# Kernel optimization log

Measured on AMD Instinct MI355X. Metric: run time of the kernel, lower is better.

## Reference

```python
import jax, jax.numpy as jnp
import numpy as np

D = 512       # d_model
M = 64        # working memory_dim
SE = 32       # episodic slots
SS = 64       # semantic slots
H = 4         # episodic heads
B, L = 2, 1024
BOT = max(D // 4, 32)  # controller bottleneck = 128


def _layernorm(x, g, b, eps=1e-5):
    mu = jnp.mean(x, axis=-1, keepdims=True)
    var = jnp.var(x, axis=-1, keepdims=True)
    return (x - mu) * jax.lax.rsqrt(var + eps) * g + b


def setup_inputs() -> dict:
    key = jax.random.key(0)
    ks = jax.random.split(key, 24)
    r = lambda i, shape, s=0.02: jax.random.normal(ks[i], shape, dtype=jnp.float32) * s
    return {
        "x": jax.random.normal(ks[0], (B, L, D), dtype=jnp.float32),
        # WorkingMemory (weights stored as (in, out))
        "Wq": r(1, (D, M)), "Wk": r(2, (D, M)), "Wv": r(3, (D, D)),
        "Wf": r(4, (D, M)), "bf": jnp.zeros((M,), jnp.float32),
        "Wo": r(5, (D, D)),
        "ln_g": jnp.ones((D,), jnp.float32), "ln_b": jnp.zeros((D,), jnp.float32),
        # EpisodicMemory
        "eslots": r(6, (1, SE, D)),
        "Eq": r(7, (D, D)), "Ek": r(8, (D, D)), "Ev": r(9, (D, D)), "Eo": r(10, (D, D)),
        # SemanticMemory
        "know": r(11, (1, SS, D)),
        "Sin": r(12, (D, D)),
        "Sg_w": r(13, (D, D)), "Sg_b": jnp.zeros((D,), jnp.float32),
        "So": r(14, (D, D)),
        # MemoryController
        "C1w": r(15, (D, BOT)), "C1b": jnp.zeros((BOT,), jnp.float32),
        "C2w": r(16, (BOT, 3)), "C2b": jnp.zeros((3,), jnp.float32),
    }


def _forward(x, Wq, Wk, Wv, Wf, bf, Wo, ln_g, ln_b,
             eslots, Eq, Ek, Ev, Eo,
             know, Sin, Sg_w, Sg_b, So,
             C1w, C1b, C2w, C2b):
    b, l, d = x.shape
    # ---- WorkingMemory (parallel gated linear attention) ----
    scale = M ** -0.5
    q = (jax.nn.elu(x @ Wq) + 1.0) * scale          # (B,L,M)
    k = jax.nn.elu(x @ Wk) + 1.0                    # (B,L,M)
    v = x @ Wv                                      # (B,L,D)
    forget = jax.nn.sigmoid(x @ Wf + bf)            # (B,L,M)
    log_f_cum = jnp.clip(jnp.cumsum(jnp.log(jnp.clip(forget, 1e-6, None)), axis=1), -20.0, 20.0)
    exp_neg = jnp.exp(-log_f_cum)
    exp_pos = jnp.exp(log_f_cum)
    kv = k[..., :, None] * v[..., None, :]          # (B,L,M,D) outer product
    cum_kv = jnp.cumsum(exp_neg[..., None] * kv, axis=1)
    Mstate = exp_pos[..., None] * cum_kv            # (B,L,M,D)
    z = exp_pos * jnp.cumsum(exp_neg * k, axis=1)   # (B,L,M)
    num = jnp.einsum('blm,blmd->bld', q, Mstate)
    den = jnp.einsum('blm,blm->bl', q, z)[..., None] + 1e-6
    w_out = _layernorm(num / den, ln_g, ln_b) @ Wo  # (B,L,D)

    # ---- EpisodicMemory (cross-attn to learned slots) ----
    hd = D // H
    mem = jnp.broadcast_to(eslots, (b, SE, D))
    qh = (x @ Eq).reshape(b, l, H, hd)
    kh = (mem @ Ek).reshape(b, SE, H, hd)
    vh = (mem @ Ev).reshape(b, SE, H, hd)
    scores = jnp.einsum('blhe,bshe->bhls', qh, kh) / jnp.sqrt(jnp.float32(hd))
    attn = jax.nn.softmax(scores, axis=-1)
    e_out = jnp.einsum('bhls,bshe->blhe', attn, vh).reshape(b, l, D) @ Eo

    # ---- SemanticMemory (single-head attn to knowledge, gated residual) ----
    kb = jnp.broadcast_to(know, (b, SS, D))
    qs = x @ Sin                                    # (B,L,D)
    s_scores = jnp.einsum('bld,bsd->bls', qs, kb) / jnp.sqrt(jnp.float32(D))
    s_attn = jax.nn.softmax(s_scores, axis=-1)
    retrieved = jnp.einsum('bls,bsd->bld', s_attn, kb)
    gate = jax.nn.sigmoid(x @ Sg_w + Sg_b)
    s_out = (gate * retrieved + (1.0 - gate) * x) @ So

    # ---- Controller fusion ----
    wts = jax.nn.softmax(jax.nn.silu(x @ C1w + C1b) @ C2w + C2b, axis=-1)  # (B,L,3)
    fused = (wts[..., 0:1] * w_out + wts[..., 1:2] * e_out + wts[..., 2:3] * s_out)
    return fused


def reference(x, Wq, Wk, Wv, Wf, bf, Wo, ln_g, ln_b,
              eslots, Eq, Ek, Ev, Eo,
              know, Sin, Sg_w, Sg_b, So,
              C1w, C1b, C2w, C2b):
    return _forward(x, Wq, Wk, Wv, Wf, bf, Wo, ln_g, ln_b,
                    eslots, Eq, Ek, Ev, Eo,
                    know, Sin, Sg_w, Sg_b, So,
                    C1w, C1b, C2w, C2b)
```

## Files before the change

kernel.cpp:

```cpp
#include <hip/hip_runtime.h>
#include <cstdint>

typedef unsigned int uint;
typedef unsigned short ushort;
typedef __attribute__((ext_vector_type(8))) short bf16x8;
typedef __attribute__((ext_vector_type(4))) float f32x4;

__device__ __forceinline__ ushort f2b(float f) {
  union { float f; uint u; } v; v.f = f;
  uint u = v.u;
  uint r = (u + 0x7FFFu + ((u >> 16) & 1u)) >> 16;
  return (ushort)r;
}
__device__ __forceinline__ float b2f(ushort h) {
  union { uint u; float f; } v; v.u = ((uint)h) << 16; return v.f;
}

__global__ __launch_bounds__(256) void k_prep(
    const float* __restrict__ x, const float* __restrict__ Wv, const float* __restrict__ Sg,
    const float* __restrict__ C1w, const float* __restrict__ Wq, const float* __restrict__ Wk,
    const float* __restrict__ Wf, const float* __restrict__ Wo, const float* __restrict__ So,
    const float* __restrict__ know, const float* __restrict__ eslots, const float* __restrict__ Ek,
    const float* __restrict__ Ev, const float* __restrict__ Sin,
    ushort* __restrict__ X16, ushort* __restrict__ Wcat, ushort* __restrict__ Wfin,
    float* __restrict__ kh, float* __restrict__ vh)
{
  __shared__ __align__(16) float pool[8320];
  int bid = blockIdx.x;
  int tid = threadIdx.x;
  int lane = tid & 63, wv = tid >> 6;

  if (bid < 128) {
    int k = bid * 4 + wv;
    const float* sp = Sin + (size_t)k * 512 + lane * 8;
    float4 s1 = *(const float4*)&sp[0];
    float4 s2 = *(const float4*)&sp[4];
    #pragma unroll 4
    for (int s = 0; s < 64; ++s) {
      const float* kp = know + (size_t)s * 512 + lane * 8;
      float4 k1 = *(const float4*)&kp[0];
      float4 k2 = *(const float4*)&kp[4];
      float part = s1.x * k1.x + s1.y * k1.y + s1.z * k1.z + s1.w * k1.w
                 + s2.x * k2.x + s2.y * k2.y + s2.z * k2.z + s2.w * k2.w;
      #pragma unroll
      for (int o = 32; o; o >>= 1) part += __shfl_xor(part, o);
      if (lane == 0) Wcat[(640 + s) * 512 + k] = f2b(part * 0.04419417382415922f);
    }
    return;
  }
  if (bid < 144) {
    float* Wt = pool;
    int b2 = bid - 128;
    int isv = b2 >= 8;
    int jb = (b2 & 7) * 64;
    const float* W = isv ? Ev : Ek;
    float* out = isv ? vh : kh;
    int jl = tid & 63, sg = tid >> 6;
    float acc[4] = {0.f, 0.f, 0.f, 0.f};
    for (int dc = 0; dc < 16; ++dc) {
      #pragma unroll
      for (int it = 0; it < 2; ++it) {
        int p = it * 256 + tid;
        int row = p >> 4, c4 = (p & 15) * 4;
        *(float4*)&Wt[row * 64 + c4] = *(const float4*)&W[(size_t)(dc * 32 + row) * 512 + jb + c4];
      }
      __syncthreads();
      #pragma unroll 8
      for (int d2 = 0; d2 < 32; ++d2) {
        float wval = Wt[d2 * 64 + jl];
        int d = dc * 32 + d2;
        acc[0] += eslots[(size_t)(sg * 4 + 0) * 512 + d] * wval;
        acc[1] += eslots[(size_t)(sg * 4 + 1) * 512 + d] * wval;
        acc[2] += eslots[(size_t)(sg * 4 + 2) * 512 + d] * wval;
        acc[3] += eslots[(size_t)(sg * 4 + 3) * 512 + d] * wval;
      }
      __syncthreads();
    }
    #pragma unroll
    for (int si = 0; si < 4; ++si)
      out[(size_t)(sg * 4 + si) * 512 + jb + jl] = acc[si];
    return;
  }
  if (bid < 440) {
    #define Tm(a,b) pool[(a) * 65 + (b)]
    int tt = bid - 144;
    const float* src; ushort* dst; int sld, dld, Nt, drow, dcol;
    if (tt < 64)       {           src = Wv;  dst = Wcat; sld = 512; dld = 512;  Nt = 8; drow = 0;    dcol = 0;   }
    else if (tt < 128) { tt -= 64; src = Sg;  dst = Wcat; sld = 512; dld = 512;  Nt = 8; drow = 704;  dcol = 0;   }
    else if (tt < 144) { tt -= 128; src = C1w; dst = Wcat; sld = 128; dld = 512; Nt = 2; drow = 1216; dcol = 0;   }
    else if (tt < 152) { tt -= 144; src = Wq;  dst = Wcat; sld = 64;  dld = 512; Nt = 1; drow = 1344; dcol = 0;   }
    else if (tt < 160) { tt -= 152; src = Wk;  dst = Wcat; sld = 64;  dld = 512; Nt = 1; drow = 1408; dcol = 0;   }
    else if (tt < 168) { tt -= 160; src = Wf;  dst = Wcat; sld = 64;  dld = 512; Nt = 1; drow = 1472; dcol = 0;   }
    else if (tt < 232) { tt -= 168; src = Wo;  dst = Wfin; sld = 512; dld = 1152; Nt = 8; drow = 0;   dcol = 0;   }
    else               { tt -= 232; src = So;  dst = Wfin; sld = 512; dld = 1152; Nt = 8; drow = 0;   dcol = 512; }
    int tk = tt / Nt, tn = tt % Nt;
    int k0 = tk * 64, n0 = tn * 64;
    int r = tid >> 4, c = (tid & 15) * 4;
    #pragma unroll
    for (int p = 0; p < 4; ++p) {
      int kk = p * 16 + r;
      float4 v = *(const float4*)&src[(size_t)(k0 + kk) * sld + n0 + c];
      Tm(c + 0, kk) = v.x; Tm(c + 1, kk) = v.y; Tm(c + 2, kk) = v.z; Tm(c + 3, kk) = v.w;
    }
    __syncthreads();
    int n = tid >> 2, kc = (tid & 3) * 16;
    uint u[8];
    #pragma unroll
    for (int j = 0; j < 8; ++j) {
      ushort lo = f2b(Tm(n, kc + 2 * j));
      ushort hi = f2b(Tm(n, kc + 2 * j + 1));
      u[j] = (uint)lo | ((uint)hi << 16);
    }
    size_t off = (size_t)(drow + n0 + n) * dld + dcol + k0 + kc;
    uint4 o1; o1.x = u[0]; o1.y = u[1]; o1.z = u[2]; o1.w = u[3];
    uint4 o2; o2.x = u[4]; o2.y = u[5]; o2.z = u[6]; o2.w = u[7];
    *(uint4*)&dst[off] = o1;
    *(uint4*)&dst[off + 8] = o2;
    #undef Tm
    return;
  }
  {
    int base = (bid - 440) * 256 + tid;
    #pragma unroll
    for (int it = 0; it < 8; ++it) {
      int t = base + it * 32768;
      float4 xv = *(const float4*)&x[(size_t)t * 4];
      uint2 o;
      o.x = (uint)f2b(xv.x) | ((uint)f2b(xv.y) << 16);
      o.y = (uint)f2b(xv.z) | ((uint)f2b(xv.w) << 16);
      *(uint2*)&X16[(size_t)t * 4] = o;
    }
  }
}

__global__ __launch_bounds__(256) void k_pre2(
    const float* __restrict__ Eq, const float* __restrict__ kh, ushort* __restrict__ Wcat)
{
  int bid = blockIdx.x;
  int tid = threadIdx.x;
  int lane = tid & 63, wv = tid >> 6;
  int gw = bid * 4 + wv;
  #pragma unroll
  for (int pp = 0; pp < 2; ++pp) {
    int pair = gw * 2 + pp;
    int k = pair >> 2, h = pair & 3;
    const float* ep = Eq + (size_t)k * 512 + h * 128 + lane * 2;
    float e0 = ep[0], e1 = ep[1];
    #pragma unroll 4
    for (int s = 0; s < 32; ++s) {
      const float* kp = kh + (size_t)s * 512 + h * 128 + lane * 2;
      float part = e0 * kp[0] + e1 * kp[1];
      #pragma unroll
      for (int o = 32; o; o >>= 1) part += __shfl_xor(part, o);
      if (lane == 0) Wcat[(512 + h * 32 + s) * 512 + k] = f2b(part * 0.08838834764831845f);
    }
  }
}

__global__ __launch_bounds__(256) void k_gemm1(
    const ushort* __restrict__ A, const ushort* __restrict__ Bw, float* __restrict__ C,
    const float* __restrict__ sgb, const float* __restrict__ c1b, const float* __restrict__ bfb)
{
  __shared__ __align__(16) ushort As[64 * 32];
  __shared__ __align__(16) ushort Bs[128 * 32];
  int tid = threadIdx.x;
  int lane = tid & 63, wv = tid >> 6;
  int wm = (wv & 1) * 32, wn = (wv >> 1) * 64;
  int lr = lane & 15, lk = lane >> 4;
  int m0 = blockIdx.y * 64, n0 = blockIdx.x * 128;
  f32x4 zero4 = {0.f, 0.f, 0.f, 0.f};
  f32x4 acc[2][4];
  #pragma unroll
  for (int a = 0; a < 2; ++a)
    #pragma unroll
    for (int b = 0; b < 4; ++b) acc[a][b] = zero4;
  for (int kt = 0; kt < 16; ++kt) {
    int k0 = kt * 32;
    {
      int p = tid, row = p >> 2, cc = p & 3;
      int cs = cc ^ ((row >> 1) & 3);
      *(uint4*)&As[p * 8] = *(const uint4*)&A[(size_t)(m0 + row) * 512 + k0 + cs * 8];
    }
    #pragma unroll
    for (int i = 0; i < 2; ++i) {
      int p = i * 256 + tid, row = p >> 2, cc = p & 3;
      int cs = cc ^ ((row >> 1) & 3);
      *(uint4*)&Bs[p * 8] = *(const uint4*)&Bw[(size_t)(n0 + row) * 512 + k0 + cs * 8];
    }
    __syncthreads();
    bf16x8 af[2], bfv[4];
    #pragma unroll
    for (int mi = 0; mi < 2; ++mi) {
      int row = wm + mi * 16 + lr;
      int cc = lk ^ ((row >> 1) & 3);
      af[mi] = *(bf16x8*)&As[row * 32 + cc * 8];
    }
    #pragma unroll
    for (int ni = 0; ni < 4; ++ni) {
      int row = wn + ni * 16 + lr;
      int cc = lk ^ ((row >> 1) & 3);
      bfv[ni] = *(bf16x8*)&Bs[row * 32 + cc * 8];
    }
    #pragma unroll
    for (int mi = 0; mi < 2; ++mi)
      #pragma unroll
      for (int ni = 0; ni < 4; ++ni)
        acc[mi][ni] = __builtin_amdgcn_mfma_f32_16x16x32_bf16(af[mi], bfv[ni], acc[mi][ni], 0, 0, 0);
    __syncthreads();
  }
  #pragma unroll
  for (int mi = 0; mi < 2; ++mi) {
    #pragma unroll
    for (int ni = 0; ni < 4; ++ni) {
      int col = n0 + wn + ni * 16 + lr;
      #pragma unroll
      for (int r = 0; r < 4; ++r) {
        int rowb = m0 + wm + mi * 16 + lk * 4 + r;
        float v = acc[mi][ni][r];
        if (col >= 704) {
          if (col < 1216) { v = 1.f / (1.f + __expf(-(v + sgb[col - 704]))); }
          else if (col < 1344) { float tt = v + c1b[col - 1216]; v = tt / (1.f + __expf(-tt)); }
          else if (col < 1408) { float e = (v > 0.f) ? v : (__expf(v) - 1.f); v = (e + 1.f) * 0.125f; }
          else if (col < 1472) { float e = (v > 0.f) ? v : (__expf(v) - 1.f); v = e + 1.f; }
          else { float logit = v + bfb[col - 1472];
                 float s = 1.f / (1.f + expf(-logit));
                 v = logf(fmaxf(s, 1e-6f)); }
        }
        C[(size_t)rowb * 1536 + col] = v;
      }
    }
  }
}

__global__ __launch_bounds__(256) void k_gemm2(
    const ushort* __restrict__ A, const ushort* __restrict__ Bw, float* __restrict__ C)
{
  __shared__ __align__(16) ushort As[64 * 32];
  __shared__ __align__(16) ushort Bs[64 * 32];
  int tid = threadIdx.x;
  int lane = tid & 63, wv = tid >> 6;
  int wm = (wv & 1) * 32, wn = (wv >> 1) * 32;
  int lr = lane & 15, lk = lane >> 4;
  int m0 = blockIdx.y * 64, n0 = blockIdx.x * 64;
  f32x4 zero4 = {0.f, 0.f, 0.f, 0.f};
  f32x4 acc[2][2];
  #pragma unroll
  for (int a = 0; a < 2; ++a)
    #pragma unroll
    for (int b = 0; b < 2; ++b) acc[a][b] = zero4;
  for (int kt = 0; kt < 36; ++kt) {
    int k0 = kt * 32;
    {
      int p = tid, row = p >> 2, cc = p & 3;
      int cs = cc ^ ((row >> 1) & 3);
      *(uint4*)&As[p * 8] = *(const uint4*)&A[(size_t)(m0 + row) * 1152 + k0 + cs * 8];
      *(uint4*)&Bs[p * 8] = *(const uint4*)&Bw[(size_t)(n0 + row) * 1152 + k0 + cs * 8];
    }
    __syncthreads();
    bf16x8 af[2], bfv[2];
    #pragma unroll
    for (int mi = 0; mi < 2; ++mi) {
      int row = wm + mi * 16 + lr;
      int cc = lk ^ ((row >> 1) & 3);
      af[mi] = *(bf16x8*)&As[row * 32 + cc * 8];
    }
    #pragma unroll
    for (int ni = 0; ni < 2; ++ni) {
      int row = wn + ni * 16 + lr;
      int cc = lk ^ ((row >> 1) & 3);
      bfv[ni] = *(bf16x8*)&Bs[row * 32 + cc * 8];
    }
    #pragma unroll
    for (int mi = 0; mi < 2; ++mi)
      #pragma unroll
      for (int ni = 0; ni < 2; ++ni)
        acc[mi][ni] = __builtin_amdgcn_mfma_f32_16x16x32_bf16(af[mi], bfv[ni], acc[mi][ni], 0, 0, 0);
    __syncthreads();
  }
  #pragma unroll
  for (int mi = 0; mi < 2; ++mi) {
    #pragma unroll
    for (int ni = 0; ni < 2; ++ni) {
      int col = n0 + wn + ni * 16 + lr;
      #pragma unroll
      for (int r = 0; r < 4; ++r) {
        int rowb = m0 + wm + mi * 16 + lk * 4 + r;
        C[(size_t)rowb * 512 + col] = acc[mi][ni][r];
      }
    }
  }
}

__global__ __launch_bounds__(256) void k_mid(
    const float* __restrict__ P,
    float* __restrict__ cn, float* __restrict__ qe, float* __restrict__ qz,
    const float* __restrict__ vh, const float* __restrict__ Eo, ushort* __restrict__ Wfin,
    const float* __restrict__ know, ushort* __restrict__ know16)
{
  __shared__ float wsumA[4];
  __shared__ float wsumB[4];
  int bid = blockIdx.x;
  int tid = threadIdx.x;
  if (bid < 128) {
    int b = bid >> 6, m = bid & 63;
    int lane = tid & 63, wv = tid >> 6;
    size_t rbase = (size_t)b * 1024 + tid * 4;

    float v0 = P[(rbase + 0) * 1536 + 1472 + m];
    float v1 = P[(rbase + 1) * 1536 + 1472 + m];
    float v2 = P[(rbase + 2) * 1536 + 1472 + m];
    float v3 = P[(rbase + 3) * 1536 + 1472 + m];
    v1 += v0; v2 += v1; v3 += v2;
    float tsum = v3;
    float sc = tsum;
    #pragma unroll
    for (int o = 1; o < 64; o <<= 1) {
      float t = __shfl_up(sc, o, 64);
      if (lane >= o) sc += t;
    }
    if (lane == 63) wsumA[wv] = sc;
    __syncthreads();
    float excl = sc - tsum;
    #pragma unroll
    for (int w2 = 0; w2 < 3; ++w2) if (w2 < wv) excl += wsumA[w2];

    float vv[4] = {v0, v1, v2, v3};
    float cv[4], qv[4];
    #pragma unroll
    for (int i = 0; i < 4; ++i) {
      size_t r = rbase + i;
      float lf = fminf(fmaxf(excl + vv[i], -20.f), 20.f);
      float en = expf(-lf), ep = expf(lf);
      float kk = P[r * 1536 + 1408 + m];
      float qq = P[r * 1536 + 1344 + m];
      cv[i] = en * kk;
      qv[i] = qq * ep;
      cn[r * 64 + m] = cv[i];
      qe[r * 64 + m] = qv[i];
    }

    float c1 = cv[0], c2 = c1 + cv[1], c3 = c2 + cv[2], c4 = c3 + cv[3];
    float t2 = c4;
    float sc2 = t2;
    #pragma unroll
    for (int o = 1; o < 64; o <<= 1) {
      float t = __shfl_up(sc2, o, 64);
      if (lane >= o) sc2 += t;
    }
    if (lane == 63) wsumB[wv] = sc2;
    __syncthreads();
    float excl2 = sc2 - t2;
    #pragma unroll
    for (int w2 = 0; w2 < 3; ++w2) if (w2 < wv) excl2 += wsumB[w2];

    float pr[4] = {c1, c2, c3, c4};
    #pragma unroll
    for (int i = 0; i < 4; ++i) {
      size_t r = rbase + i;
      qz[r * 64 + m] = qv[i] * (excl2 + pr[i]);
    }
    return;
  }
  if (bid < 384) {
    int o = (bid - 128) * 256 + tid;
    int hs = o >> 9, j = o & 511;
    int h = hs >> 5, s = hs & 31;
    const float* vhp = vh + (size_t)s * 512 + h * 128;
    float acc = 0.f;
    #pragma unroll 16
    for (int e = 0; e < 128; ++e) acc += vhp[e] * Eo[(size_t)(h * 128 + e) * 512 + j];
    Wfin[(size_t)j * 1152 + 1024 + hs] = f2b(acc);
    return;
  }
  {
    int t = (bid - 384) * 256 + tid;
    #pragma unroll
    for (int j = 0; j < 2; ++j) {
      float4 v = *(const float4*)&know[(size_t)t * 8 + j * 4];
      uint2 o;
      o.x = (uint)f2b(v.x) | ((uint)f2b(v.y) << 16);
      o.y = (uint)f2b(v.z) | ((uint)f2b(v.w) << 16);
      *(uint2*)&know16[(size_t)t * 8 + j * 4] = o;
    }
  }
}

__global__ __launch_bounds__(256) void k_scanA(
    const float* __restrict__ cn, const float* __restrict__ P, float* __restrict__ Send)
{
  __shared__ __align__(16) float cnS[32 * 64];
  __shared__ __align__(16) float vS[16 * 64];
  int tid = threadIdx.x;
  int bid = blockIdx.x;
  int dt = bid & 7, c = (bid >> 3) & 31, b = bid >> 8;
  int rb0 = b * 1024 + c * 32;
  #pragma unroll
  for (int it = 0; it < 2; ++it) {
    int p = it * 256 + tid;
    int row = p >> 4, c4f = (p & 15) * 4;
    *(float4*)&cnS[row * 64 + c4f] = *(const float4*)&cn[(size_t)(rb0 + row) * 64 + c4f];
  }
  __syncthreads();
  int mg = tid >> 4, dl = tid & 15;
  float4 acc[4];
  #pragma unroll
  for (int i = 0; i < 4; ++i) acc[i] = make_float4(0.f, 0.f, 0.f, 0.f);
  for (int ig = 0; ig < 2; ++ig) {
    int rb = rb0 + ig * 16;
    int row = tid >> 4, c4f = (tid & 15) * 4;
    *(float4*)&vS[row * 64 + c4f] = *(const float4*)&P[(size_t)(rb + row) * 1536 + dt * 64 + c4f];
    __syncthreads();
    #pragma unroll 4
    for (int i = 0; i < 16; ++i) {
      float4 vv = *(float4*)&vS[i * 64 + dl * 4];
      float4 cm = *(float4*)&cnS[(ig * 16 + i) * 64 + mg * 4];
      acc[0].x += cm.x * vv.x; acc[0].y += cm.x * vv.y; acc[0].z += cm.x * vv.z; acc[0].w += cm.x * vv.w;
      acc[1].x += cm.y * vv.x; acc[1].y += cm.y * vv.y; acc[1].z += cm.y * vv.z; acc[1].w += cm.y * vv.w;
      acc[2].x += cm.z * vv.x; acc[2].y += cm.z * vv.y; acc[2].z += cm.z * vv.z; acc[2].w += cm.z * vv.w;
      acc[3].x += cm.w * vv.x; acc[3].y += cm.w * vv.y; acc[3].z += cm.w * vv.z; acc[3].w += cm.w * vv.w;
    }
    __syncthreads();
  }
  #pragma unroll
  for (int mi = 0; mi < 4; ++mi) {
    int m = mg * 4 + mi;
    *(float4*)&Send[(size_t)((b * 32 + c) * 64 + m) * 512 + dt * 64 + dl * 4] = acc[mi];
  }
}

__global__ __launch_bounds__(256) void k_scanB(const float* __restrict__ Send, float* __restrict__ carry)
{
  int t = blockIdx.x * 256 + threadIdx.x;
  int d = t & 511, m = (t >> 9) & 63, b = t >> 15;
  float run = 0.f;
  #pragma unroll 8
  for (int c = 0; c < 32; ++c) {
    size_t idx = (size_t)((b * 32 + c) * 64 + m) * 512 + d;
    carry[idx] = run;
    run += Send[idx];
  }
}

__global__ __launch_bounds__(256) void k_scanC(
    const float* __restrict__ cn, const float* __restrict__ qe, const float* __restrict__ P,
    const float* __restrict__ carry, float* __restrict__ num)
{
  __shared__ __align__(16) float cnS[32 * 64];
  __shared__ __align__(16) float qeS[32 * 64];
  __shared__ __align__(16) float vS[16 * 64];
  int tid = threadIdx.x;
  int bid = blockIdx.x;
  int dt = bid & 7, c = (bid >> 3) & 31, b = bid >> 8;
  int rb0 = b * 1024 + c * 32;
  #pragma unroll
  for (int it = 0; it < 2; ++it) {
    int p = it * 256 + tid;
    int row = p >> 4, c4f = (p & 15) * 4;
    *(float4*)&cnS[row * 64 + c4f] = *(const float4*)&cn[(size_t)(rb0 + row) * 64 + c4f];
    *(float4*)&qeS[row * 64 + c4f] = *(const float4*)&qe[(size_t)(rb0 + row) * 64 + c4f];
  }
  int mg = tid & 3, dl = tid >> 2;
  int d = dt * 64 + dl;
  float S[16];
  #pragma unroll
  for (int mi = 0; mi < 16; ++mi)
    S[mi] = carry[(size_t)((b * 32 + c) * 64 + mg * 16 + mi) * 512 + d];
  __syncthreads();
  for (int ig = 0; ig < 2; ++ig) {
    int rb = rb0 + ig * 16;
    int row = tid >> 4, c4f = (tid & 15) * 4;
    *(float4*)&vS[row * 64 + c4f] = *(const float4*)&P[(size_t)(rb + row) * 1536 + dt * 64 + c4f];
    __syncthreads();
    for (int i = 0; i < 16; ++i) {
      int ii = ig * 16 + i;
      float vv = vS[i * 64 + dl];
      float p = 0.f;
      #pragma unroll
      for (int j = 0; j < 4; ++j) {
        float4 c4 = *(float4*)&cnS[ii * 64 + mg * 16 + j * 4];
        float4 q4 = *(float4*)&qeS[ii * 64 + mg * 16 + j * 4];
        S[j * 4 + 0] += c4.x * vv; p += q4.x * S[j * 4 + 0];
        S[j * 4 + 1] += c4.y * vv; p += q4.y * S[j * 4 + 1];
        S[j * 4 + 2] += c4.z * vv; p += q4.z * S[j * 4 + 2];
        S[j * 4 + 3] += c4.w * vv; p += q4.w * S[j * 4 + 3];
      }
      p += __shfl_xor(p, 1);
      p += __shfl_xor(p, 2);
      if (mg == 0) num[(size_t)(rb0 + ii) * 512 + d] = p;
    }
    __syncthreads();
  }
}

__global__ __launch_bounds__(256) void k_post(
    const float* __restrict__ P, const float* __restrict__ x,
    const float* __restrict__ num, const float* __restrict__ qz,
    const ushort* __restrict__ know16, const float* __restrict__ lng,
    const float* __restrict__ lnb, const float* __restrict__ C2w,
    const float* __restrict__ C2b, ushort* __restrict__ Afin)
{
  __shared__ __align__(16) ushort kbuf[32 * 512];
  __shared__ float attnL[4][64];
  __shared__ float w2L[4];
  int tid = threadIdx.x;
  int w = tid >> 6, lane = tid & 63;
  int r0 = blockIdx.x * 4;
  int r = r0 + w;
  size_t pr = (size_t)r * 1536;

  float h0 = P[pr + 1216 + lane], h1 = P[pr + 1280 + lane];
  float a0 = h0 * C2w[lane * 3 + 0] + h1 * C2w[(64 + lane) * 3 + 0];
  float a1 = h0 * C2w[lane * 3 + 1] + h1 * C2w[(64 + lane) * 3 + 1];
  float a2 = h0 * C2w[lane * 3 + 2] + h1 * C2w[(64 + lane) * 3 + 2];
  #pragma unroll
  for (int o = 32; o; o >>= 1) {
    a0 += __shfl_xor(a0, o); a1 += __shfl_xor(a1, o); a2 += __shfl_xor(a2, o);
  }
  a0 += C2b[0]; a1 += C2b[1]; a2 += C2b[2];
  float mxc = fmaxf(a0, fmaxf(a1, a2));
  float e0 = expf(a0 - mxc), e1 = expf(a1 - mxc), e2c = expf(a2 - mxc);
  float inv = 1.f / (e0 + e1 + e2c);
  float w0 = e0 * inv, w1 = e1 * inv, w2 = e2c * inv;
  if (lane == 0) w2L[w] = w2;

  {
    float den = qz[(size_t)r * 64 + lane];
    #pragma unroll
    for (int o = 32; o; o >>= 1) den += __shfl_xor(den, o);
    den += 1e-6f;
    float y[8];
    float4 n0 = *(const float4*)&num[(size_t)r * 512 + lane * 8];
    float4 n1 = *(const float4*)&num[(size_t)r * 512 + lane * 8 + 4];
    y[0] = n0.x / den; y[1] = n0.y / den; y[2] = n0.z / den; y[3] = n0.w / den;
    y[4] = n1.x / den; y[5] = n1.y / den; y[6] = n1.z / den; y[7] = n1.w / den;
    float s1 = 0.f, s2 = 0.f;
    #pragma unroll
    for (int i = 0; i < 8; ++i) { s1 += y[i]; s2 += y[i] * y[i]; }
    #pragma unroll
    for (int o = 32; o; o >>= 1) { s1 += __shfl_xor(s1, o); s2 += __shfl_xor(s2, o); }
    float mu = s1 * (1.f / 512.f);
    float var = s2 * (1.f / 512.f) - mu * mu;
    float rs = rsqrtf(var + 1e-5f);
    uint4 outv;
    uint pk[4];
    #pragma unroll
    for (int p2 = 0; p2 < 4; ++p2) {
      float o0 = (y[2 * p2] - mu) * rs * lng[lane * 8 + 2 * p2] + lnb[lane * 8 + 2 * p2];
      float o1 = (y[2 * p2 + 1] - mu) * rs * lng[lane * 8 + 2 * p2 + 1] + lnb[lane * 8 + 2 * p2 + 1];
      pk[p2] = (uint)f2b(o0 * w0) | ((uint)f2b(o1 * w0) << 16);
    }
    outv.x = pk[0]; outv.y = pk[1]; outv.z = pk[2]; outv.w = pk[3];
    *(uint4*)&Afin[(size_t)r * 1152 + lane * 8] = outv;
  }

  {
    int h = lane >> 4, ei = (lane & 15) * 2;
    float v0 = P[pr + 512 + h * 32 + ei], v1 = P[pr + 512 + h * 32 + ei + 1];
    float mxe = fmaxf(v0, v1);
    #pragma unroll
    for (int o = 1; o < 16; o <<= 1) mxe = fmaxf(mxe, __shfl_xor(mxe, o));
    float ee0 = __expf(v0 - mxe), ee1 = __expf(v1 - mxe);
    float ss = ee0 + ee1;
    #pragma unroll
    for (int o = 1; o < 16; o <<= 1) ss += __shfl_xor(ss, o);
    float sc1 = w1 / ss;
    uint pkv = (uint)f2b(ee0 * sc1) | ((uint)f2b(ee1 * sc1) << 16);
    *(uint*)&Afin[(size_t)r * 1152 + 1024 + h * 32 + ei] = pkv;
  }

  {
    float lv = P[pr + 640 + lane];
    float mx = lv;
    #pragma unroll
    for (int o = 32; o; o >>= 1) mx = fmaxf(mx, __shfl_xor(mx, o));
    float e = __expf(lv - mx);
    float sum = e;
    #pragma unroll
    for (int o = 32; o; o >>= 1) sum += __shfl_xor(sum, o);
    attnL[w][lane] = e / sum;
  }
  __syncthreads();

  int dd = tid * 2;
  float acc[4][2];
  #pragma unroll
  for (int i = 0; i < 4; ++i) { acc[i][0] = 0.f; acc[i][1] = 0.f; }
  for (int hs = 0; hs < 2; ++hs) {
    #pragma unroll
    for (int i = 0; i < 8; ++i) {
      int idx = i * 256 + tid;
      *(uint4*)&kbuf[idx * 8] = *(const uint4*)&know16[(size_t)hs * 16384 + idx * 8];
    }
    __syncthreads();
    for (int s = 0; s < 32; ++s) {
      uint uu = *(uint*)&kbuf[s * 512 + dd];
      float k0 = b2f((ushort)(uu & 0xffff));
      float k1 = b2f((ushort)(uu >> 16));
      #pragma unroll
      for (int row = 0; row < 4; ++row) {
        float a = attnL[row][hs * 32 + s];
        acc[row][0] += a * k0;
        acc[row][1] += a * k1;
      }
    }
    __syncthreads();
  }
  #pragma unroll
  for (int row = 0; row < 4; ++row) {
    int rr = r0 + row;
    float g0 = P[(size_t)rr * 1536 + 704 + dd];
    float g1 = P[(size_t)rr * 1536 + 704 + dd + 1];
    float x0 = x[(size_t)rr * 512 + dd], x1 = x[(size_t)rr * 512 + dd + 1];
    float w2v = w2L[row];
    float m0 = g0 * acc[row][0] + (1.f - g0) * x0;
    float m1 = g1 * acc[row][1] + (1.f - g1) * x1;
    uint pkv = (uint)f2b(w2v * m0) | ((uint)f2b(w2v * m1) << 16);
    *(uint*)&Afin[(size_t)rr * 1152 + 512 + dd] = pkv;
  }
}

extern "C" void kernel_launch(void* const* d_in, const int* in_sizes, int n_in,
                              void* d_out, int out_size, void* d_ws, size_t ws_size,
                              hipStream_t stream)
{
  const float* x     = (const float*)d_in[0];
  const float* Wq    = (const float*)d_in[1];
  const float* Wk    = (const float*)d_in[2];
  const float* Wv    = (const float*)d_in[3];
  const float* Wf    = (const float*)d_in[4];
  const float* bfb   = (const float*)d_in[5];
  const float* Wo    = (const float*)d_in[6];
  const float* ln_g  = (const float*)d_in[7];
  const float* ln_b  = (const float*)d_in[8];
  const float* eslots= (const float*)d_in[9];
  const float* Eq    = (const float*)d_in[10];
  const float* Ek    = (const float*)d_in[11];
  const float* Ev    = (const float*)d_in[12];
  const float* Eo    = (const float*)d_in[13];
  const float* know  = (const float*)d_in[14];
  const float* Sin   = (const float*)d_in[15];
  const float* Sg_w  = (const float*)d_in[16];
  const float* Sg_b  = (const float*)d_in[17];
  const float* So    = (const float*)d_in[18];
  const float* C1w   = (const float*)d_in[19];
  const float* C1b   = (const float*)d_in[20];
  const float* C2w   = (const float*)d_in[21];
  const float* C2b   = (const float*)d_in[22];

  char* ws = (char*)d_ws;
  ushort* X16    = (ushort*)(ws + 0);
  ushort* Wcat   = (ushort*)(ws + 2097152);
  ushort* Wfin   = (ushort*)(ws + 3670016);
  ushort* know16 = (ushort*)(ws + 4849664);
  float*  kh     = (float*)(ws + 4915200);
  float*  vh     = (float*)(ws + 4980736);
  float*  P      = (float*)(ws + 5046272);
  float*  cn     = (float*)(ws + 18153472);
  float*  qe     = (float*)(ws + 18677760);
  float*  qz     = (float*)(ws + 19202048);
  float*  Send   = (float*)(ws + 19726336);
  float*  carry  = (float*)(ws + 28114944);
  float*  num    = (float*)(ws + 36503552);
  ushort* Afin   = (ushort*)(ws + 40697856);

  k_prep<<<dim3(568), dim3(256), 0, stream>>>(x, Wv, Sg_w, C1w, Wq, Wk, Wf, Wo, So, know,
                                              eslots, Ek, Ev, Sin,
                                              X16, Wcat, Wfin, kh, vh);
  k_pre2<<<dim3(256), dim3(256), 0, stream>>>(Eq, kh, Wcat);
  k_gemm1<<<dim3(12, 32), dim3(256), 0, stream>>>(X16, Wcat, P, Sg_b, C1b, bfb);
  k_mid<<<dim3(400), dim3(256), 0, stream>>>(P, cn, qe, qz, vh, Eo, Wfin, know, know16);
  k_scanA<<<dim3(512), dim3(256), 0, stream>>>(cn, P, Send);
  k_scanB<<<dim3(256), dim3(256), 0, stream>>>(Send, carry);
  k_scanC<<<dim3(512), dim3(256), 0, stream>>>(cn, qe, P, carry, num);
  k_post<<<dim3(512), dim3(256), 0, stream>>>(P, x, num, qz, know16, ln_g, ln_b, C2w, C2b, Afin);
  k_gemm2<<<dim3(8, 32), dim3(256), 0, stream>>>(Afin, Wfin, (float*)d_out);
}
```

Measured before the change: 146.8 us.

## Split prep kernel and spread small weight-folding matmuls across more blocks

The monolithic prep kernel is split in two. The first kernel handles the Sin·know fold with half the slots per wave, doubling the block count, and computes the eslots·Ek/Ev projections one output per thread over 128 blocks instead of 16 blocks with LDS tiling. The second kernel does the transpose/bf16 conversion work with a smaller LDS pool. The aim is to remove the long serial tail from the few heavy blocks, at the cost of an extra launch and uncached strided reads of the weight columns.

```diff
diff --git a/kernel.cpp b/kernel.cpp
--- a/kernel.cpp
+++ b/kernel.cpp
@@ -16,27 +16,24 @@
   union { uint u; float f; } v; v.u = ((uint)h) << 16; return v.f;
 }
 
-__global__ __launch_bounds__(256) void k_prep(
-    const float* __restrict__ x, const float* __restrict__ Wv, const float* __restrict__ Sg,
-    const float* __restrict__ C1w, const float* __restrict__ Wq, const float* __restrict__ Wk,
-    const float* __restrict__ Wf, const float* __restrict__ Wo, const float* __restrict__ So,
-    const float* __restrict__ know, const float* __restrict__ eslots, const float* __restrict__ Ek,
-    const float* __restrict__ Ev, const float* __restrict__ Sin,
-    ushort* __restrict__ X16, ushort* __restrict__ Wcat, ushort* __restrict__ Wfin,
-    float* __restrict__ kh, float* __restrict__ vh)
-{
-  __shared__ __align__(16) float pool[8320];
+__global__ __launch_bounds__(256) void k_prepA(
+    const float* __restrict__ know, const float* __restrict__ eslots,
+    const float* __restrict__ Ek, const float* __restrict__ Ev, const float* __restrict__ Sin,
+    ushort* __restrict__ Wcat, float* __restrict__ kh, float* __restrict__ vh)
+{
   int bid = blockIdx.x;
   int tid = threadIdx.x;
   int lane = tid & 63, wv = tid >> 6;
 
-  if (bid < 128) {
-    int k = bid * 4 + wv;
+  if (bid < 256) {
+    int k = bid * 2 + (wv >> 1);
+    int s0 = (wv & 1) * 32;
     const float* sp = Sin + (size_t)k * 512 + lane * 8;
     float4 s1 = *(const float4*)&sp[0];
     float4 s2 = *(const float4*)&sp[4];
     #pragma unroll 4
-    for (int s = 0; s < 64; ++s) {
+    for (int si = 0; si < 32; ++si) {
+      int s = s0 + si;
       const float* kp = know + (size_t)s * 512 + lane * 8;
       float4 k1 = *(const float4*)&kp[0];
       float4 k2 = *(const float4*)&kp[4];
@@ -48,42 +45,38 @@
     }
     return;
   }
-  if (bid < 144) {
-    float* Wt = pool;
-    int b2 = bid - 128;
-    int isv = b2 >= 8;
-    int jb = (b2 & 7) * 64;
+  {
+    int t = (bid - 256) * 256 + tid;
+    int isv = (t >= 16384);
+    int o = t & 16383; int s = o >> 9, j = o & 511;
     const float* W = isv ? Ev : Ek;
-    float* out = isv ? vh : kh;
-    int jl = tid & 63, sg = tid >> 6;
-    float acc[4] = {0.f, 0.f, 0.f, 0.f};
-    for (int dc = 0; dc < 16; ++dc) {
-      #pragma unroll
-      for (int it = 0; it < 2; ++it) {
-        int p = it * 256 + tid;
-        int row = p >> 4, c4 = (p & 15) * 4;
-        *(float4*)&Wt[row * 64 + c4] = *(const float4*)&W[(size_t)(dc * 32 + row) * 512 + jb + c4];
-      }
-      __syncthreads();
-      #pragma unroll 8
-      for (int d2 = 0; d2 < 32; ++d2) {
-        float wval = Wt[d2 * 64 + jl];
-        int d = dc * 32 + d2;
-        acc[0] += eslots[(size_t)(sg * 4 + 0) * 512 + d] * wval;
-        acc[1] += eslots[(size_t)(sg * 4 + 1) * 512 + d] * wval;
-        acc[2] += eslots[(size_t)(sg * 4 + 2) * 512 + d] * wval;
-        acc[3] += eslots[(size_t)(sg * 4 + 3) * 512 + d] * wval;
-      }
-      __syncthreads();
-    }
-    #pragma unroll
-    for (int si = 0; si < 4; ++si)
-      out[(size_t)(sg * 4 + si) * 512 + jb + jl] = acc[si];
-    return;
-  }
-  if (bid < 440) {
+    const float* es = eslots + (size_t)s * 512;
+    float a0 = 0.f, a1 = 0.f, a2 = 0.f, a3 = 0.f;
+    #pragma unroll 8
+    for (int d = 0; d < 512; d += 4) {
+      a0 += es[d + 0] * W[(size_t)(d + 0) * 512 + j];
+      a1 += es[d + 1] * W[(size_t)(d + 1) * 512 + j];
+      a2 += es[d + 2] * W[(size_t)(d + 2) * 512 + j];
+      a3 += es[d + 3] * W[(size_t)(d + 3) * 512 + j];
+    }
+    float acc = (a0 + a1) + (a2 + a3);
+    (isv ? vh : kh)[(size_t)s * 512 + j] = acc;
+  }
+}
+
+__global__ __launch_bounds__(256) void k_prepB(
+    const float* __restrict__ x, const float* __restrict__ Wv, const float* __restrict__ Sg,
+    const float* __restrict__ C1w, const float* __restrict__ Wq, const float* __restrict__ Wk,
+    const float* __restrict__ Wf, const float* __restrict__ Wo, const float* __restrict__ So,
+    ushort* __restrict__ X16, ushort* __restrict__ Wcat, ushort* __restrict__ Wfin)
+{
+  __shared__ __align__(16) float pool[4160];
+  int bid = blockIdx.x;
+  int tid = threadIdx.x;
+
+  if (bid < 296) {
     #define Tm(a,b) pool[(a) * 65 + (b)]
-    int tt = bid - 144;
+    int tt = bid;
     const float* src; ushort* dst; int sld, dld, Nt, drow, dcol;
     if (tt < 64)       {           src = Wv;  dst = Wcat; sld = 512; dld = 512;  Nt = 8; drow = 0;    dcol = 0;   }
     else if (tt < 128) { tt -= 64; src = Sg;  dst = Wcat; sld = 512; dld = 512;  Nt = 8; drow = 704;  dcol = 0;   }
@@ -120,7 +113,7 @@
     return;
   }
   {
-    int base = (bid - 440) * 256 + tid;
+    int base = (bid - 296) * 256 + tid;
     #pragma unroll
     for (int it = 0; it < 8; ++it) {
       int t = base + it * 32768;
@@ -663,9 +656,9 @@
   float*  num    = (float*)(ws + 36503552);
   ushort* Afin   = (ushort*)(ws + 40697856);
 
-  k_prep<<<dim3(568), dim3(256), 0, stream>>>(x, Wv, Sg_w, C1w, Wq, Wk, Wf, Wo, So, know,
-                                              eslots, Ek, Ev, Sin,
-                                              X16, Wcat, Wfin, kh, vh);
+  k_prepA<<<dim3(384), dim3(256), 0, stream>>>(know, eslots, Ek, Ev, Sin, Wcat, kh, vh);
+  k_prepB<<<dim3(424), dim3(256), 0, stream>>>(x, Wv, Sg_w, C1w, Wq, Wk, Wf, Wo, So,
+                                               X16, Wcat, Wfin);
   k_pre2<<<dim3(256), dim3(256), 0, stream>>>(Eq, kh, Wcat);
   k_gemm1<<<dim3(12, 32), dim3(256), 0, stream>>>(X16, Wcat, P, Sg_b, C1b, bfb);
   k_mid<<<dim3(400), dim3(256), 0, stream>>>(P, cn, qe, qz, vh, Eo, Wfin, know, know16);
```

After: 136.6 us. -7.0%, faster.
